# Kernel optimization log

Measured on AMD Instinct MI355X. Metric: run time of the kernel, lower is better.

## Reference

```python
import jax, jax.numpy as jnp
import numpy as np

DIM = 16            # Hilbert space dimension
D = DIM * DIM       # superoperator / vectorized-density dimension (256)
N_TS = 128          # number of timesteps
N_CTRLS = 2         # number of control fields
DT = 0.02           # timestep
SQUARINGS = 6       # scaling-and-squaring steps for matrix_exp
TAYLOR_TERMS = 12   # Taylor (Horner) order for matrix_exp


def setup_inputs() -> dict:
    key = jax.random.key(0)
    ks = jax.random.split(key, 12)
    s = 0.05  # keep generator norms small so expm(A*dt) is well-conditioned
    D2 = (D, D)
    ctrls_real = jax.random.normal(ks[0], (N_TS, N_CTRLS), jnp.float32)
    ctrls_im = jax.random.normal(ks[1], (N_TS, N_CTRLS), jnp.float32)
    dyn_gen_re = s * jax.random.normal(ks[2], D2, jnp.float32)
    dyn_gen_im = s * jax.random.normal(ks[3], D2, jnp.float32)
    ctrl_gen_re = s * jax.random.normal(ks[4], (N_CTRLS, 2, D, D), jnp.float32)
    ctrl_gen_im = s * jax.random.normal(ks[5], (N_CTRLS, 2, D, D), jnp.float32)
    # initial / target: vectorized density-like states (identity/DIM + noise)
    eye_vec = (jnp.eye(DIM, dtype=jnp.float32) / DIM).reshape(D)
    initial_re = eye_vec + 0.01 * jax.random.normal(ks[6], (D,), jnp.float32)
    initial_im = 0.01 * jax.random.normal(ks[7], (D,), jnp.float32)
    target_re = eye_vec + 0.01 * jax.random.normal(ks[8], (D,), jnp.float32)
    target_im = 0.01 * jax.random.normal(ks[9], (D,), jnp.float32)
    return dict(ctrls_real=ctrls_real, ctrls_im=ctrls_im,
                dyn_gen_re=dyn_gen_re, dyn_gen_im=dyn_gen_im,
                ctrl_gen_re=ctrl_gen_re, ctrl_gen_im=ctrl_gen_im,
                initial_re=initial_re, initial_im=initial_im,
                target_re=target_re, target_im=target_im)


def _expm(A):
    """Differentiable matrix exponential: scaling-and-squaring + Taylor (Horner)."""
    A = A / (2.0 ** SQUARINGS)
    I = jnp.eye(A.shape[-1], dtype=A.dtype)
    R = I
    for k in range(TAYLOR_TERMS, 0, -1):
        R = I + (A @ R) / k
    for _ in range(SQUARINGS):
        R = R @ R
    return R


def _evolve(cr, ci, dyn, Gr, Gi, s0):
    # control generators: _get_ctrl_gen -> cr*(G0+G1) + 1j*ci*(G0-G1)
    G0 = Gr[:, 0] + 1j * Gi[:, 0]   # [n_ctrls, D, D]
    G1 = Gr[:, 1] + 1j * Gi[:, 1]
    Gp = G0 + G1
    Gm = G0 - G1
    crc = cr.astype(Gp.dtype)
    cic = ci.astype(Gm.dtype)
    # per-timestep dynamics generator A_k = dyn + sum_j ctrl terms  [n_ts, D, D]
    A = (dyn[None, :, :]
         + jnp.einsum('kj,jab->kab', crc, Gp)
         + 1j * jnp.einsum('kj,jab->kab', cic, Gm))
    props = jax.vmap(_expm)(A * DT)  # [n_ts, D, D]
    diag_idx = jnp.arange(DIM) * (DIM + 1)  # trace indices of vec(rho)

    def step(s, P):
        s = P @ s
        s = s / s[diag_idx].sum()  # trace normalization
        return s, None

    sT, _ = jax.lax.scan(step, s0, props)
    return sT


def reference(ctrls_real, ctrls_im, dyn_gen_re, dyn_gen_im,
              ctrl_gen_re, ctrl_gen_im, initial_re, initial_im,
              target_re, target_im):
    dyn = dyn_gen_re + 1j * dyn_gen_im
    s0 = initial_re + 1j * initial_im
    sT = _evolve(ctrls_real, ctrls_im, dyn, ctrl_gen_re, ctrl_gen_im, s0)
    tgt = target_re + 1j * target_im
    fid_err = jnp.linalg.norm((sT - tgt).reshape(DIM, DIM))  # Frobenius norm
    return sT, fid_err
```

## Files before the change

### kernel.cpp

```cpp
#include <hip/hip_runtime.h>
#include <math.h>

#define DD    256
#define PLQ   65536
#define SLOTB 131072
#define NTS   128
#define DT_C  0.02f

typedef unsigned short u16;
typedef unsigned int   u32;
typedef __attribute__((ext_vector_type(8))) short s16x8;
typedef __attribute__((ext_vector_type(4))) float f32x4;

typedef __attribute__((address_space(1))) const unsigned int GU32;
typedef __attribute__((address_space(3))) unsigned int LU32;

__device__ __forceinline__ u32 swzB(u32 b) {
    return b ^ (((((b >> 7) ^ (b >> 10)) & 7u)) << 4);
}
__device__ __forceinline__ u16 f2bf(float f) {
    u32 u = __float_as_uint(f);
    return (u16)((u + 0x7FFFu + ((u >> 16) & 1u)) >> 16);
}
__device__ __forceinline__ float bf2f(u16 h) {
    return __uint_as_float(((u32)h) << 16);
}
__device__ __forceinline__ void gll16(const u16* g, char* ldsBase, u32 ldsByteOff) {
    u32 off = (u32)__builtin_amdgcn_readfirstlane((int)ldsByteOff);
    __builtin_amdgcn_global_load_lds((GU32*)g, (LU32*)(ldsBase + off), 16, 0, 0);
}

__global__ __launch_bounds__(256)
void build_kernel(const float* __restrict__ cr, const float* __restrict__ ci,
                  const float* __restrict__ dre, const float* __restrict__ dimg,
                  const float* __restrict__ gre, const float* __restrict__ gim,
                  u16* __restrict__ Xn, int ts0)
{
    const int ts = blockIdx.y;
    const int k  = ts0 + ts;
    const int i4 = (blockIdx.x * 256 + threadIdx.x) * 4;

    const float c0f = cr[2*k], c1f = cr[2*k+1];
    const float e0f = ci[2*k], e1f = ci[2*k+1];

    const float4 g0r = *(const float4*)&gre[0*PLQ + i4];
    const float4 g1r = *(const float4*)&gre[1*PLQ + i4];
    const float4 g2r = *(const float4*)&gre[2*PLQ + i4];
    const float4 g3r = *(const float4*)&gre[3*PLQ + i4];
    const float4 g0i = *(const float4*)&gim[0*PLQ + i4];
    const float4 g1i = *(const float4*)&gim[1*PLQ + i4];
    const float4 g2i = *(const float4*)&gim[2*PLQ + i4];
    const float4 g3i = *(const float4*)&gim[3*PLQ + i4];
    const float4 d_r = *(const float4*)&dre[i4];
    const float4 d_i = *(const float4*)&dimg[i4];
    const float* gr00 = &g0r.x; const float* gr01 = &g1r.x;
    const float* gr10 = &g2r.x; const float* gr11 = &g3r.x;
    const float* gi00 = &g0i.x; const float* gi01 = &g1i.x;
    const float* gi10 = &g2i.x; const float* gi11 = &g3i.x;
    const float* dr4  = &d_r.x; const float* di4  = &d_i.x;

    ushort4 hr, hi;
    u16* hrp = &hr.x; u16* hip = &hi.x;
    #pragma unroll
    for (int j = 0; j < 4; ++j) {
        const float are = dr4[j] + c0f*(gr00[j]+gr01[j]) + c1f*(gr10[j]+gr11[j])
                                 - e0f*(gi00[j]-gi01[j]) - e1f*(gi10[j]-gi11[j]);
        const float aim = di4[j] + c0f*(gi00[j]+gi01[j]) + c1f*(gi10[j]+gi11[j])
                                 + e0f*(gr00[j]-gr01[j]) + e1f*(gr10[j]-gr11[j]);
        hrp[j] = f2bf(DT_C * are);
        hip[j] = f2bf(DT_C * aim);
    }
    u16* X = Xn + (size_t)ts * SLOTB;
    *(ushort4*)&X[i4]       = hr;
    *(ushort4*)&X[PLQ + i4] = hi;
}

__global__ __launch_bounds__(256)
void cgemm64(const u16* __restrict__ Ab, const u16* __restrict__ Bb,
             u16* __restrict__ outN,
             const u16* __restrict__ X1b, const u16* __restrict__ X2b,
             float aN, float bN1, float bN2,
             int aS, int aO, int bS, int bO, int cS, int cO,
             int x1S, int x1O, int x2S, int x2O)
{
    __shared__ char lds[32768];

    const u32 nwg = 16u * (u32)gridDim.z;
    const u32 wg  = (u32)blockIdx.x + 4u*(u32)blockIdx.y + 16u*(u32)blockIdx.z;
    const u32 q   = nwg >> 3;
    const u32 w   = (wg & 7u) * q + (wg >> 3);
    const int bn = (int)(w & 3u) * 64;
    const int bm = (int)((w >> 2) & 3u) * 64;
    const int z  = (int)(w >> 4);

    const u16* __restrict__ A = Ab + (size_t)(z*aS + aO) * SLOTB;
    const u16* __restrict__ B = Bb + (size_t)(z*bS + bO) * SLOTB;

    const int t = threadIdx.x;

    const u32 b0 = (u32)t * 16u, b1 = 4096u + (u32)t * 16u;
    const u32 L0 = swzB(b0),     L1 = swzB(b1);
    const int rA0 = (int)(L0 >> 7), kA0 = (int)((L0 & 127u) >> 1);
    const int rA1 = (int)(L1 >> 7), kA1 = (int)((L1 & 127u) >> 1);
    const u32 wvoff = ((u32)(t >> 6)) * 1024u;

    const u16* pA0 = A + (size_t)(bm + rA0)*DD + kA0;
    const u16* pA1 = A + (size_t)(bm + rA1)*DD + kA1;

    const int kRow = t >> 3;
    const int nCh  = t & 7;

    const int wv = t >> 6, ln = t & 63;
    const int wrow = (wv >> 1) * 32, wcol = (wv & 1) * 32;
    const int lg = ln >> 4, lc = ln & 15;

    f32x4 accR[2][2], accI[2][2];
    #pragma unroll
    for (int i = 0; i < 2; ++i)
        #pragma unroll
        for (int j = 0; j < 2; ++j) {
            accR[i][j] = (f32x4){0.f,0.f,0.f,0.f};
            accI[i][j] = (f32x4){0.f,0.f,0.f,0.f};
        }

    {
        gll16(pA0,       lds, wvoff +     0u);
        gll16(pA1,       lds, wvoff +  4096u);
        gll16(pA0 + PLQ, lds, wvoff +  8192u);
        gll16(pA1 + PLQ, lds, wvoff + 12288u);
        #pragma unroll
        for (int h = 0; h < 2; ++h) {
            const int kk = h*32 + kRow;
            const s16x8 vr = *(const s16x8*)(B +       (size_t)kk*DD + bn + nCh*8);
            const s16x8 vi = *(const s16x8*)(B + PLQ + (size_t)kk*DD + bn + nCh*8);
            #pragma unroll
            for (int e = 0; e < 8; ++e) {
                const u32 off = swzB((u32)(nCh*8 + e)*128u + (u32)kk*2u);
                *(u16*)(lds + 16384 + off) = (u16)vr[e];
                *(u16*)(lds + 24576 + off) = (u16)vi[e];
            }
        }
    }
    __syncthreads();

    for (int it = 0; it < 4; ++it) {
        s16x8 nvr0, nvi0, nvr1, nvi1;
        if (it < 3) {
            const int k1 = 64*(it + 1);
            nvr0 = *(const s16x8*)(B +       (size_t)(k1 + kRow)*DD + bn + nCh*8);
            nvi0 = *(const s16x8*)(B + PLQ + (size_t)(k1 + kRow)*DD + bn + nCh*8);
            nvr1 = *(const s16x8*)(B +       (size_t)(k1 + 32 + kRow)*DD + bn + nCh*8);
            nvi1 = *(const s16x8*)(B + PLQ + (size_t)(k1 + 32 + kRow)*DD + bn + nCh*8);
        }

        #pragma unroll
        for (int s = 0; s < 2; ++s) {
            s16x8 ar[2], ai[2], br[2], bi[2];
            #pragma unroll
            for (int fm = 0; fm < 2; ++fm) {
                const u32 so = swzB((u32)(wrow + fm*16 + lc)*128u + (u32)(s*4 + lg)*16u);
                ar[fm] = *(const s16x8*)(lds + so);
                ai[fm] = *(const s16x8*)(lds + 8192 + so);
            }
            #pragma unroll
            for (int fn = 0; fn < 2; ++fn) {
                const u32 so = swzB((u32)(wcol + fn*16 + lc)*128u + (u32)(s*4 + lg)*16u);
                br[fn] = *(const s16x8*)(lds + 16384 + so);
                bi[fn] = *(const s16x8*)(lds + 24576 + so);
            }
            #pragma unroll
            for (int fm = 0; fm < 2; ++fm)
                #pragma unroll
                for (int fn = 0; fn < 2; ++fn) {
                    accI[fm][fn] = __builtin_amdgcn_mfma_f32_16x16x32_bf16(ar[fm], bi[fn], accI[fm][fn], 0, 0, 0);
                    accI[fm][fn] = __builtin_amdgcn_mfma_f32_16x16x32_bf16(ai[fm], br[fn], accI[fm][fn], 0, 0, 0);
                }
            #pragma unroll
            for (int fm = 0; fm < 2; ++fm) ai[fm] ^= (short)0x8000u;
            #pragma unroll
            for (int fm = 0; fm < 2; ++fm)
                #pragma unroll
                for (int fn = 0; fn < 2; ++fn) {
                    accR[fm][fn] = __builtin_amdgcn_mfma_f32_16x16x32_bf16(ar[fm], br[fn], accR[fm][fn], 0, 0, 0);
                    accR[fm][fn] = __builtin_amdgcn_mfma_f32_16x16x32_bf16(ai[fm], bi[fn], accR[fm][fn], 0, 0, 0);
                }
        }

        if (it < 3) {
            const int k1 = 64*(it + 1);
            __syncthreads();
            gll16(pA0 + k1,       lds, wvoff +     0u);
            gll16(pA1 + k1,       lds, wvoff +  4096u);
            gll16(pA0 + PLQ + k1, lds, wvoff +  8192u);
            gll16(pA1 + PLQ + k1, lds, wvoff + 12288u);
            #pragma unroll
            for (int e = 0; e < 8; ++e) {
                const u32 off0 = swzB((u32)(nCh*8 + e)*128u + (u32)kRow*2u);
                const u32 off1 = swzB((u32)(nCh*8 + e)*128u + (u32)(32 + kRow)*2u);
                *(u16*)(lds + 16384 + off0) = (u16)nvr0[e];
                *(u16*)(lds + 24576 + off0) = (u16)nvi0[e];
                *(u16*)(lds + 16384 + off1) = (u16)nvr1[e];
                *(u16*)(lds + 24576 + off1) = (u16)nvi1[e];
            }
            __syncthreads();
        }
    }

    __syncthreads();
    #pragma unroll
    for (int fm = 0; fm < 2; ++fm)
        #pragma unroll
        for (int fn = 0; fn < 2; ++fn) {
            const int rb = wrow + fm*16 + lg*4;
            const int c  = wcol + fn*16 + lc;
            #pragma unroll
            for (int j = 0; j < 4; ++j) {
                const u32 ob = swzB((u32)(rb + j)*128u + (u32)c*2u);
                *(u16*)(lds +        ob) = f2bf(aN * accR[fm][fn][j]);
                *(u16*)(lds + 8192 + ob) = f2bf(aN * accI[fm][fn][j]);
            }
        }
    __syncthreads();

    u16* oN = outN + (size_t)(z*cS + cO) * SLOTB;
    const u16* x1 = X1b ? X1b + (size_t)(z*x1S + x1O) * SLOTB : nullptr;
    const u16* x2 = X2b ? X2b + (size_t)(z*x2S + x2O) * SLOTB : nullptr;

    const int orow = t >> 2;
    const u32 och  = ((u32)t & 3u) * 32u;
    const size_t gOff = (size_t)(bm + orow)*DD + bn + (och >> 1);

    #pragma unroll
    for (int pl = 0; pl < 2; ++pl) {
        const u32 lb   = (u32)pl * 8192u + (u32)orow * 128u + och;
        const size_t g = gOff + (size_t)pl * PLQ;
        #pragma unroll
        for (int h = 0; h < 2; ++h) {
            const s16x8 cv = *(const s16x8*)(lds + swzB(lb + (u32)h*16u));
            float o[8];
            #pragma unroll
            for (int e = 0; e < 8; ++e) o[e] = bf2f((u16)cv[e]);
            if (x1) {
                const s16x8 xv = *(const s16x8*)(x1 + g + h*8);
                #pragma unroll
                for (int e = 0; e < 8; ++e) o[e] += bN1 * bf2f((u16)xv[e]);
            }
            if (x2) {
                const s16x8 xv = *(const s16x8*)(x2 + g + h*8);
                #pragma unroll
                for (int e = 0; e < 8; ++e) o[e] += bN2 * bf2f((u16)xv[e]);
            }
            s16x8 ov;
            #pragma unroll
            for (int e = 0; e < 8; ++e) ov[e] = (short)f2bf(o[e]);
            *(s16x8*)(oN + g + h*8) = ov;
        }
    }
}

__global__ __launch_bounds__(256)
void final_kernel(const u16* __restrict__ Et,
                  const float* __restrict__ s0r, const float* __restrict__ s0i,
                  const float* __restrict__ tgr, const float* __restrict__ tgi,
                  float* __restrict__ out, int outSize)
{
    __shared__ float sr[DD], si[DD], red[DD];
    __shared__ float cR, cI;
    const int t = threadIdx.x;
    sr[t] = s0r[t];
    si[t] = s0i[t];
    __syncthreads();

    const u16* Er = Et + (size_t)t*DD;
    const u16* Ei = Er + PLQ;
    float ar = sr[t], ai = si[t];
    for (int kk = 0; kk < DD/8; ++kk) {
        const s16x8 er = *(const s16x8*)(Er + kk*8);
        const s16x8 ei = *(const s16x8*)(Ei + kk*8);
        #pragma unroll
        for (int jj = 0; jj < 8; ++jj) {
            const float pr = bf2f((u16)er[jj]);
            const float pi = bf2f((u16)ei[jj]);
            const int k = kk*8 + jj;
            ar += pr*sr[k] - pi*si[k];
            ai += pr*si[k] + pi*sr[k];
        }
    }
    __syncthreads();
    sr[t] = ar; si[t] = ai;
    __syncthreads();

    if (t == 0) {
        float xr = 0.f, xi = 0.f;
        for (int i = 0; i < 16; ++i) { xr += sr[i*17]; xi += si[i*17]; }
        cR = xr; cI = xi;
    }
    __syncthreads();

    const float den = cR*cR + cI*cI;
    const float str = (ar*cR + ai*cI) / den;
    const float sti = (ai*cR - ar*cI) / den;

    const float dr = str - tgr[t];
    const float di = sti - tgi[t];
    red[t] = dr*dr + di*di;
    __syncthreads();
    for (int s = 128; s > 0; s >>= 1) {
        if (t < s) red[t] += red[t + s];
        __syncthreads();
    }
    const float fid = sqrtf(red[0]);

    if (outSize >= 2*DD + 1) {
        out[2*t] = str; out[2*t+1] = sti;
        if (t == 0) out[2*DD] = fid;
    } else if (outSize == 2*DD) {
        out[2*t] = str; out[2*t+1] = sti;
    } else {
        out[t] = str;
        if (t == 0 && outSize > DD) out[DD] = fid;
    }
}

extern "C" void kernel_launch(void* const* d_in, const int* in_sizes, int n_in,
                              void* d_out, int out_size, void* d_ws, size_t ws_size,
                              hipStream_t stream)
{
    (void)in_sizes; (void)n_in;
    const float* cr   = (const float*)d_in[0];
    const float* ci   = (const float*)d_in[1];
    const float* dre  = (const float*)d_in[2];
    const float* dimg = (const float*)d_in[3];
    const float* gre  = (const float*)d_in[4];
    const float* gim  = (const float*)d_in[5];
    const float* s0r  = (const float*)d_in[6];
    const float* s0i  = (const float*)d_in[7];
    const float* tgr  = (const float*)d_in[8];
    const float* tgi  = (const float*)d_in[9];

    const float c2 = 0.5f, c3i = 1.f/6.f;

    u16* ws = (u16*)d_ws;
    const long slots = (long)(ws_size / 2) / SLOTB;

    if (slots >= 384) {
        u16* RX = ws;
        u16* R1 = ws + 128L * SLOTB;
        u16* R2 = ws + 256L * SLOTB;

        build_kernel<<<dim3(PLQ/1024, 128), 256, 0, stream>>>(
            cr, ci, dre, dimg, gre, gim, RX, 0);

        const dim3 g128(4, 4, 128);
        cgemm64<<<g128, 256, 0, stream>>>(RX, RX, R1, nullptr, nullptr,
            1.f, 0.f, 0.f,
            1,0, 1,0, 1,0, 0,0, 0,0);
        cgemm64<<<g128, 256, 0, stream>>>(R1, RX, R2, RX, R1,
            c3i, 1.f, c2,
            1,0, 1,0, 1,0, 1,0, 1,0);

        u16* cur = R2;
        u16* oth = R1;
        for (int n = 128; n > 1; n >>= 1) {
            cgemm64<<<dim3(4, 4, n/2), 256, 0, stream>>>(
                cur, cur, oth, cur, cur,
                1.f, 1.f, 1.f,
                2,1, 2,0, 1,0, 2,1, 2,0);
            u16* tmp = cur; cur = oth; oth = tmp;
        }
        final_kernel<<<1, 256, 0, stream>>>(cur, s0r, s0i, tgr, tgi,
                                            (float*)d_out, out_size);
    } else {
        u16* P  = ws;
        u16* CB = ws + 128L * SLOTB;
        int C = (int)((slots - 128) / 2);
        if (C > NTS) C = NTS;
        if (C < 32)  C = 32;

        for (int ts0 = 0; ts0 < NTS; ts0 += C) {
            int nb = NTS - ts0; if (nb > C) nb = C;
            u16* Xn = CB;
            u16* P2 = CB + 1L*C*SLOTB;

            build_kernel<<<dim3(PLQ/1024, nb), 256, 0, stream>>>(
                cr, ci, dre, dimg, gre, gim, Xn, ts0);

            const dim3 grid(4, 4, nb);
            cgemm64<<<grid, 256, 0, stream>>>(Xn, Xn, P2, nullptr, nullptr,
                1.f, 0.f, 0.f,
                1,0, 1,0, 1,0, 0,0, 0,0);
            cgemm64<<<grid, 256, 0, stream>>>(P2, Xn, P, Xn, P2,
                c3i, 1.f, c2,
                1,0, 1,0, 1,ts0, 1,0, 1,0);
        }

        u16* cur = P;
        u16* oth = CB;
        for (int n = 128; n > 1; n >>= 1) {
            cgemm64<<<dim3(4, 4, n/2), 256, 0, stream>>>(
                cur, cur, oth, cur, cur,
                1.f, 1.f, 1.f,
                2,1, 2,0, 1,0, 2,1, 2,0);
            u16* tmp = cur; cur = oth; oth = tmp;
        }
        final_kernel<<<1, 256, 0, stream>>>(cur, s0r, s0i, tgr, tgi,
                                            (float*)d_out, out_size);
    }
}
```

Before: 177.6 us.

## Stop product tree at four matrices and apply them via matvecs in final kernel

The pairwise product-tree reduction now stops when four propagator products remain instead of one. The final kernel applies those four matrices to the state vector one after another as matrix-vector products, using 1024 threads that split the K dimension four ways. This drops the last two tree levels, whose tiny GEMM launches had little parallelism. cgemm64 also gains a min-blocks-per-CU hint in launch_bounds, which may limit its registers.

```diff
diff --git a/kernel.cpp b/kernel.cpp
--- a/kernel.cpp
+++ b/kernel.cpp
@@ -75,7 +75,7 @@
     *(ushort4*)&X[PLQ + i4] = hi;
 }
 
-__global__ __launch_bounds__(256)
+__global__ __launch_bounds__(256, 8)
 void cgemm64(const u16* __restrict__ Ab, const u16* __restrict__ Bb,
              u16* __restrict__ outN,
              const u16* __restrict__ X1b, const u16* __restrict__ X2b,
@@ -258,37 +258,52 @@
     }
 }
 
-__global__ __launch_bounds__(256)
-void final_kernel(const u16* __restrict__ Et,
-                  const float* __restrict__ s0r, const float* __restrict__ s0i,
-                  const float* __restrict__ tgr, const float* __restrict__ tgi,
-                  float* __restrict__ out, int outSize)
+__global__ __launch_bounds__(1024)
+void final4_kernel(const u16* __restrict__ Es, int nE,
+                   const float* __restrict__ s0r, const float* __restrict__ s0i,
+                   const float* __restrict__ tgr, const float* __restrict__ tgi,
+                   float* __restrict__ out, int outSize)
 {
-    __shared__ float sr[DD], si[DD], red[DD];
+    __shared__ float sr[DD], si[DD];
+    __shared__ float psr[4][DD], psi[4][DD];
+    __shared__ float red[DD];
     __shared__ float cR, cI;
-    const int t = threadIdx.x;
-    sr[t] = s0r[t];
-    si[t] = s0i[t];
-    __syncthreads();
-
-    const u16* Er = Et + (size_t)t*DD;
-    const u16* Ei = Er + PLQ;
-    float ar = sr[t], ai = si[t];
-    for (int kk = 0; kk < DD/8; ++kk) {
-        const s16x8 er = *(const s16x8*)(Er + kk*8);
-        const s16x8 ei = *(const s16x8*)(Ei + kk*8);
-        #pragma unroll
-        for (int jj = 0; jj < 8; ++jj) {
-            const float pr = bf2f((u16)er[jj]);
-            const float pi = bf2f((u16)ei[jj]);
-            const int k = kk*8 + jj;
-            ar += pr*sr[k] - pi*si[k];
-            ai += pr*si[k] + pi*sr[k];
-        }
-    }
-    __syncthreads();
-    sr[t] = ar; si[t] = ai;
-    __syncthreads();
+
+    const int t   = threadIdx.x;
+    const int row = t & 255;
+    const int qt  = t >> 8;
+
+    if (t < DD) { sr[t] = s0r[t]; si[t] = s0i[t]; }
+    __syncthreads();
+
+    for (int j = 0; j < nE; ++j) {
+        const u16* Er = Es + (size_t)j*SLOTB + (size_t)row*DD + qt*64;
+        const u16* Ei = Er + PLQ;
+        float ar = 0.f, ai = 0.f;
+        #pragma unroll
+        for (int kk = 0; kk < 8; ++kk) {
+            const s16x8 er = *(const s16x8*)(Er + kk*8);
+            const s16x8 ei = *(const s16x8*)(Ei + kk*8);
+            #pragma unroll
+            for (int e = 0; e < 8; ++e) {
+                const int k = qt*64 + kk*8 + e;
+                const float pr = bf2f((u16)er[e]);
+                const float pi = bf2f((u16)ei[e]);
+                ar += pr*sr[k] - pi*si[k];
+                ai += pr*si[k] + pi*sr[k];
+            }
+        }
+        psr[qt][row] = ar; psi[qt][row] = ai;
+        __syncthreads();
+        float nr = 0.f, ni = 0.f;
+        if (t < DD) {
+            nr = sr[t] + psr[0][t] + psr[1][t] + psr[2][t] + psr[3][t];
+            ni = si[t] + psi[0][t] + psi[1][t] + psi[2][t] + psi[3][t];
+        }
+        __syncthreads();
+        if (t < DD) { sr[t] = nr; si[t] = ni; }
+        __syncthreads();
+    }
 
     if (t == 0) {
         float xr = 0.f, xi = 0.f;
@@ -298,12 +313,14 @@
     __syncthreads();
 
     const float den = cR*cR + cI*cI;
-    const float str = (ar*cR + ai*cI) / den;
-    const float sti = (ai*cR - ar*cI) / den;
-
-    const float dr = str - tgr[t];
-    const float di = sti - tgi[t];
-    red[t] = dr*dr + di*di;
+    float str = 0.f, sti = 0.f;
+    if (t < DD) {
+        str = (sr[t]*cR + si[t]*cI) / den;
+        sti = (si[t]*cR - sr[t]*cI) / den;
+        const float dr = str - tgr[t];
+        const float di = sti - tgi[t];
+        red[t] = dr*dr + di*di;
+    }
     __syncthreads();
     for (int s = 128; s > 0; s >>= 1) {
         if (t < s) red[t] += red[t + s];
@@ -311,14 +328,16 @@
     }
     const float fid = sqrtf(red[0]);
 
-    if (outSize >= 2*DD + 1) {
-        out[2*t] = str; out[2*t+1] = sti;
-        if (t == 0) out[2*DD] = fid;
-    } else if (outSize == 2*DD) {
-        out[2*t] = str; out[2*t+1] = sti;
-    } else {
-        out[t] = str;
-        if (t == 0 && outSize > DD) out[DD] = fid;
+    if (t < DD) {
+        if (outSize >= 2*DD + 1) {
+            out[2*t] = str; out[2*t+1] = sti;
+            if (t == 0) out[2*DD] = fid;
+        } else if (outSize == 2*DD) {
+            out[2*t] = str; out[2*t+1] = sti;
+        } else {
+            out[t] = str;
+            if (t == 0 && outSize > DD) out[DD] = fid;
+        }
     }
 }
 
@@ -361,15 +380,15 @@
 
         u16* cur = R2;
         u16* oth = R1;
-        for (int n = 128; n > 1; n >>= 1) {
+        for (int n = 128; n > 4; n >>= 1) {
             cgemm64<<<dim3(4, 4, n/2), 256, 0, stream>>>(
                 cur, cur, oth, cur, cur,
                 1.f, 1.f, 1.f,
                 2,1, 2,0, 1,0, 2,1, 2,0);
             u16* tmp = cur; cur = oth; oth = tmp;
         }
-        final_kernel<<<1, 256, 0, stream>>>(cur, s0r, s0i, tgr, tgi,
-                                            (float*)d_out, out_size);
+        final4_kernel<<<1, 1024, 0, stream>>>(cur, 4, s0r, s0i, tgr, tgi,
+                                              (float*)d_out, out_size);
     } else {
         u16* P  = ws;
         u16* CB = ws + 128L * SLOTB;
@@ -396,14 +415,14 @@
 
         u16* cur = P;
         u16* oth = CB;
-        for (int n = 128; n > 1; n >>= 1) {
+        for (int n = 128; n > 4; n >>= 1) {
             cgemm64<<<dim3(4, 4, n/2), 256, 0, stream>>>(
                 cur, cur, oth, cur, cur,
                 1.f, 1.f, 1.f,
                 2,1, 2,0, 1,0, 2,1, 2,0);
             u16* tmp = cur; cur = oth; oth = tmp;
         }
-        final_kernel<<<1, 256, 0, stream>>>(cur, s0r, s0i, tgr, tgi,
-                                            (float*)d_out, out_size);
-    }
-}
+        final4_kernel<<<1, 1024, 0, stream>>>(cur, 4, s0r, s0i, tgr, tgi,
+                                              (float*)d_out, out_size);
+    }
+}
```

New measurement: 184.8 us. 1.04x slower.
